# Kernel optimization log

Hardware: AMD Instinct MI355X
Metric: run time of the kernel (lower is better)

The kernel has to match this reference:

```python
import jax, jax.numpy as jnp
import numpy as np

B, H, W = 64, 256, 256
G = 64
V = G * G          # 4096
HID = 512
S = 50


def _conv(x, w, b):
    # x: (B,C,H,W), w: (O,I,3,3) -> 'same' conv, NCHW
    y = jax.lax.conv_general_dilated(x, w, (1, 1), 'SAME',
                                     dimension_numbers=('NCHW', 'OIHW', 'NCHW'))
    return y + b[None, :, None, None]


def setup_inputs() -> dict:
    key = jax.random.key(0)
    ks = jax.random.split(key, 14)

    def lin(k, shape, fan_in):
        return (jax.random.normal(k, shape, jnp.float32) / np.float32(np.sqrt(fan_in)))

    return {
        'mask': jax.random.uniform(ks[0], (B, 1, H, W), jnp.float32),
        'target_ids': jax.random.randint(ks[1], (B, S), 0, V),
        'conv1_w': lin(ks[2], (16, 1, 3, 3), 9), 'conv1_b': jnp.zeros((16,), jnp.float32),
        'conv2_w': lin(ks[3], (32, 16, 3, 3), 16 * 9), 'conv2_b': jnp.zeros((32,), jnp.float32),
        'feat_w': lin(ks[4], (HID, 32), 32), 'feat_b': jnp.zeros((HID,), jnp.float32),
        'ctx_w': lin(ks[5], (HID, HID), HID), 'ctx_b': jnp.zeros((HID,), jnp.float32),
        'tok_emb': jax.random.normal(ks[6], (V + 1, HID), jnp.float32) * 0.02,
        'w_ih': lin(ks[7], (4 * HID, HID), HID), 'w_hh': lin(ks[8], (4 * HID, HID), HID),
        'b_ih': jnp.zeros((4 * HID,), jnp.float32), 'b_hh': jnp.zeros((4 * HID,), jnp.float32),
        'head_w': lin(ks[9], (V, HID), HID), 'head_b': jnp.zeros((V,), jnp.float32),
    }


def reference(mask, target_ids, conv1_w, conv1_b, conv2_w, conv2_b,
              feat_w, feat_b, ctx_w, ctx_b, tok_emb,
              w_ih, w_hh, b_ih, b_hh, head_w, head_b):
    b = mask.shape[0]
    vocab = head_w.shape[0]

    # --- CNN encoder ---
    x = jax.nn.relu(_conv(mask, conv1_w, conv1_b))                    # (B,16,H,W)
    x = jax.lax.reduce_window(x, -jnp.inf, jax.lax.max,
                              (1, 1, 2, 2), (1, 1, 2, 2), 'VALID')    # (B,16,H/2,W/2)
    x = jax.nn.relu(_conv(x, conv2_w, conv2_b))                       # (B,32,H/2,W/2)
    x = x.mean(axis=(2, 3))                                           # AdaptiveAvgPool2d(1) -> (B,32)

    h0 = x @ feat_w.T + feat_b                                        # (B,HID)
    c0 = jnp.zeros_like(h0)
    ctx = h0 @ ctx_w.T + ctx_b                                        # (B,HID)

    # Full teacher forcing (ratio=1.0): input token at t=0 is start token V,
    # at t>0 it is target_ids[:, t-1]. All embeddings gathered upfront.
    start = jnp.full((b, 1), vocab, dtype=target_ids.dtype)
    toks = jnp.concatenate([start, target_ids[:, :-1]], axis=1)       # (B,S)
    embs = tok_emb[toks]                                              # (B,S,HID)
    lstm_in = jnp.swapaxes(embs, 0, 1) + ctx[None]                    # (S,B,HID)

    bias = b_ih + b_hh

    def step(carry, inp):
        h, c = carry
        gates = inp @ w_ih.T + h @ w_hh.T + bias                      # (B,4*HID)
        i, f, g, o = jnp.split(gates, 4, axis=-1)
        c = jax.nn.sigmoid(f) * c + jax.nn.sigmoid(i) * jnp.tanh(g)
        h = jax.nn.sigmoid(o) * jnp.tanh(c)
        logit = h @ head_w.T + head_b                                 # (B,V)
        return (h, c), logit

    _, logits = jax.lax.scan(step, (h0, c0), lstm_in)                 # (S,B,V)
    return jnp.swapaxes(logits, 0, 1)                                 # (B,S,V)
```

## Files before the change

### kernel.cpp

```cpp
#include <hip/hip_runtime.h>
#include <cmath>

typedef __attribute__((ext_vector_type(8))) _Float16 f16x8;
typedef __attribute__((ext_vector_type(2))) _Float16 f16x2;
typedef __attribute__((ext_vector_type(4))) float f32x4;
typedef __attribute__((ext_vector_type(4))) unsigned u32x4;

#define LSTM_NB 32

__device__ __forceinline__ unsigned short f2h(float x) {
  return __builtin_bit_cast(unsigned short, (_Float16)x);
}

__device__ __forceinline__ float dot2(unsigned a, unsigned b, float c) {
#if __has_builtin(__builtin_amdgcn_fdot2)
  return __builtin_amdgcn_fdot2(__builtin_bit_cast(f16x2, a),
                                __builtin_bit_cast(f16x2, b), c, false);
#else
  f16x2 av = __builtin_bit_cast(f16x2, a), bv = __builtin_bit_cast(f16x2, b);
  return fmaf((float)av[0], (float)bv[0], fmaf((float)av[1], (float)bv[1], c));
#endif
}

__device__ __forceinline__ void gload16(const void* g, void* l) {
  __builtin_amdgcn_global_load_lds(
      (const __attribute__((address_space(1))) void*)g,
      (__attribute__((address_space(3))) void*)l, 16, 0, 0);
}

__device__ __forceinline__ void cload16(const void* p, u32x4* dst) {
  asm volatile("global_load_dwordx4 %0, %1, off sc0 sc1"
               : "=v"(*dst)
               : "v"(p));
}

__global__ __launch_bounds__(512) void k_conv(
    const float* __restrict__ mask, const float* __restrict__ w1,
    const float* __restrict__ b1, const float* __restrict__ w2,
    const float* __restrict__ b2, float* __restrict__ part)
{
  __shared__ unsigned s_p1p[8][18 * 36];
  __shared__ unsigned s_w2p[32][8][9];
  __shared__ float s_w1[144];
  __shared__ float s_b1[16];
  __shared__ float s_b2[32];

  const int tid = threadIdx.x;
  const int b = blockIdx.x >> 5;
  const int tile = blockIdx.x & 31;
  const int px0 = (tile & 3) * 32, py0 = (tile >> 2) * 16;
  const float* mb = mask + (size_t)b * 65536;

  for (int i = tid; i < 144; i += 512) s_w1[i] = w1[i];
  for (int i = tid; i < 2304; i += 512) {
    int oc = i / 72, p8 = (i % 72) / 9, k = i % 9;
    unsigned lo = f2h(w2[(size_t)(oc * 16 + 2 * p8) * 9 + k]);
    unsigned hi = f2h(w2[(size_t)(oc * 16 + 2 * p8 + 1) * 9 + k]);
    s_w2p[oc][p8][k] = lo | (hi << 16);
  }
  if (tid < 16) s_b1[tid] = b1[tid];
  if (tid < 32) s_b2[tid] = b2[tid];
  __syncthreads();

  for (int idx = tid; idx < 18 * 34; idx += 512) {
    int ly = idx / 34, lx = idx - ly * 34;
    int py = py0 - 1 + ly, px = px0 - 1 + lx;
    if (py < 0 || py >= 128 || px < 0 || px >= 128) {
      for (int p8 = 0; p8 < 8; p8++) s_p1p[p8][ly * 36 + lx] = 0;
    } else {
      float patch[4][4];
      int gy0 = 2 * py - 1, gx0 = 2 * px - 1;
#pragma unroll
      for (int i = 0; i < 4; i++) {
        int gy = gy0 + i;
        bool yok = (gy >= 0 && gy < 256);
#pragma unroll
        for (int j = 0; j < 4; j++) {
          int gx = gx0 + j;
          patch[i][j] = (yok && gx >= 0 && gx < 256) ? mb[gy * 256 + gx] : 0.f;
        }
      }
      float m[16];
      for (int o = 0; o < 16; o++) {
        float mm = 0.f;
#pragma unroll
        for (int dy = 0; dy < 2; dy++)
#pragma unroll
          for (int dx = 0; dx < 2; dx++) {
            float v = s_b1[o];
#pragma unroll
            for (int ky = 0; ky < 3; ky++)
#pragma unroll
              for (int kx = 0; kx < 3; kx++)
                v = fmaf(patch[dy + ky][dx + kx], s_w1[o * 9 + ky * 3 + kx], v);
            mm = fmaxf(mm, v);
          }
        m[o] = mm;
      }
#pragma unroll
      for (int p8 = 0; p8 < 8; p8++)
        s_p1p[p8][ly * 36 + lx] =
            (unsigned)f2h(m[2 * p8]) | ((unsigned)f2h(m[2 * p8 + 1]) << 16);
    }
  }
  __syncthreads();

  const int ocg = tid >> 6;
  const int sp = tid & 63;
  const int sx = (sp & 7) * 4, sy = (sp >> 3) * 2;
  float acc[4][8];
#pragma unroll
  for (int a = 0; a < 4; a++)
#pragma unroll
    for (int q = 0; q < 8; q++) acc[a][q] = 0.f;

  for (int p8 = 0; p8 < 8; p8++) {
    unsigned pp[4][6];
#pragma unroll
    for (int i = 0; i < 4; i++) {
      const unsigned* row = &s_p1p[p8][(sy + i) * 36 + sx];
#pragma unroll
      for (int j = 0; j < 6; j++) pp[i][j] = row[j];
    }
#pragma unroll
    for (int o4 = 0; o4 < 4; o4++) {
      const unsigned* w = &s_w2p[ocg * 4 + o4][p8][0];
      unsigned w00 = w[0], w01 = w[1], w02 = w[2];
      unsigned w10 = w[3], w11 = w[4], w12 = w[5];
      unsigned w20 = w[6], w21 = w[7], w22 = w[8];
#pragma unroll
      for (int y = 0; y < 2; y++)
#pragma unroll
        for (int x = 0; x < 4; x++) {
          float s = acc[o4][y * 4 + x];
          s = dot2(pp[y][x], w00, s);
          s = dot2(pp[y][x + 1], w01, s);
          s = dot2(pp[y][x + 2], w02, s);
          s = dot2(pp[y + 1][x], w10, s);
          s = dot2(pp[y + 1][x + 1], w11, s);
          s = dot2(pp[y + 1][x + 2], w12, s);
          s = dot2(pp[y + 2][x], w20, s);
          s = dot2(pp[y + 2][x + 1], w21, s);
          s = dot2(pp[y + 2][x + 2], w22, s);
          acc[o4][y * 4 + x] = s;
        }
    }
  }

  const int lane = tid & 63;
#pragma unroll
  for (int o4 = 0; o4 < 4; o4++) {
    float bv = s_b2[ocg * 4 + o4];
    float s = 0.f;
#pragma unroll
    for (int q = 0; q < 8; q++) s += fmaxf(acc[o4][q] + bv, 0.f);
    for (int off = 32; off > 0; off >>= 1) s += __shfl_down(s, off, 64);
    if (lane == 0) part[(b * 32 + tile) * 32 + ocg * 4 + o4] = s;
  }
}

__global__ __launch_bounds__(256) void k_pool_ctx(
    const float* __restrict__ part, const float* __restrict__ feat_w,
    const float* __restrict__ feat_b, const float* __restrict__ ctx_w,
    const float* __restrict__ ctx_b, float* __restrict__ h0,
    unsigned short* __restrict__ h0f, float* __restrict__ ctx)
{
  const int b = blockIdx.x, tid = threadIdx.x;
  __shared__ float pl[32];
  __shared__ float hs[512];
  if (tid < 32) {
    float s = 0.f;
    for (int t = 0; t < 32; t++) s += part[(b * 32 + t) * 32 + tid];
    pl[tid] = s * (1.0f / 16384.0f);
  }
  __syncthreads();
  for (int j = tid; j < 512; j += 256) {
    float acc = feat_b[j];
    const float* w = feat_w + j * 32;
#pragma unroll
    for (int ic = 0; ic < 32; ic++) acc = fmaf(pl[ic], w[ic], acc);
    h0[b * 512 + j] = acc;
    h0f[b * 512 + j] = f2h(acc);
    hs[j] = acc;
  }
  __syncthreads();
  for (int j = tid; j < 512; j += 256) {
    const float* w = ctx_w + (size_t)j * 512;
    float s0 = 0.f, s1 = 0.f, s2 = 0.f, s3 = 0.f;
    for (int k = 0; k < 512; k += 4) {
      float4 w4 = *(const float4*)(w + k);
      s0 = fmaf(hs[k], w4.x, s0);
      s1 = fmaf(hs[k + 1], w4.y, s1);
      s2 = fmaf(hs[k + 2], w4.z, s2);
      s3 = fmaf(hs[k + 3], w4.w, s3);
    }
    ctx[b * 512 + j] = ctx_b[j] + ((s0 + s1) + (s2 + s3));
  }
}

__global__ __launch_bounds__(256) void k_prep(
    const float* __restrict__ wih, const float* __restrict__ hw,
    unsigned short* __restrict__ wihb, unsigned short* __restrict__ hwb,
    int* __restrict__ flags)
{
  const int i = blockIdx.x * 256 + threadIdx.x;
  if (i < 1600) flags[i] = 0;
  if (i < 262144) {
    float4 v = *(const float4*)(wih + (size_t)i * 4);
    unsigned lo = (unsigned)f2h(v.x) | ((unsigned)f2h(v.y) << 16);
    unsigned hi = (unsigned)f2h(v.z) | ((unsigned)f2h(v.w) << 16);
    *(uint2*)(wihb + (size_t)i * 4) = make_uint2(lo, hi);
  } else if (i < 786432) {
    const int j = i - 262144;
    float4 v = *(const float4*)(hw + (size_t)j * 4);
    unsigned lo = (unsigned)f2h(v.x) | ((unsigned)f2h(v.y) << 16);
    unsigned hi = (unsigned)f2h(v.z) | ((unsigned)f2h(v.w) << 16);
    *(uint2*)(hwb + (size_t)j * 4) = make_uint2(lo, hi);
  }
}

__global__ __launch_bounds__(256) void k_zero_f(float* __restrict__ p) {
  p[blockIdx.x * 256 + threadIdx.x] = 0.f;
}

__global__ __launch_bounds__(128) void k_build_A(
    const float* __restrict__ tok_emb, const int* __restrict__ tgt,
    const float* __restrict__ ctx, unsigned short* __restrict__ A)
{
  const int r = blockIdx.x;
  const int t = r >> 6, b = r & 63;
  const int tok = (t == 0) ? 4096 : tgt[b * 50 + (t - 1)];
  const int i = threadIdx.x * 4;
  float4 ev = *(const float4*)(tok_emb + (size_t)tok * 512 + i);
  float4 cv = *(const float4*)(ctx + b * 512 + i);
  unsigned lo = (unsigned)f2h(ev.x + cv.x) | ((unsigned)f2h(ev.y + cv.y) << 16);
  unsigned hi = (unsigned)f2h(ev.z + cv.z) | ((unsigned)f2h(ev.w + cv.w) << 16);
  *(uint2*)(A + (size_t)r * 512 + i) = make_uint2(lo, hi);
}

template <int MODE>
__global__ __launch_bounds__(256) void k_gemm_mfma(
    const unsigned short* __restrict__ A, const unsigned short* __restrict__ B,
    const float* __restrict__ bias_a, const float* __restrict__ bias_b,
    float* __restrict__ C, int NB)
{
  __shared__ unsigned short sA[128 * 32];
  __shared__ unsigned short sB[128 * 32];
  const int tid = threadIdx.x;
  const int bx = blockIdx.x % NB, by = blockIdx.x / NB;
  const int lane = tid & 63, wv = tid >> 6;
  const int wr = wv >> 1, wc = wv & 1;
  const unsigned short* Ab = A + (size_t)by * 128 * 512;
  const unsigned short* Bb = B + (size_t)bx * 128 * 512;

  f32x4 acc[4][4];
#pragma unroll
  for (int m = 0; m < 4; m++)
#pragma unroll
    for (int n = 0; n < 4; n++) acc[m][n] = (f32x4){0.f, 0.f, 0.f, 0.f};

  const int r0 = tid >> 2, c0 = (tid & 3) * 8;
  const int idx1 = tid + 256;
  const int r1 = idx1 >> 2, c1 = (idx1 & 3) * 8;
  unsigned short* lA0 = sA + (size_t)wv * 512;
  unsigned short* lA1 = sA + 2048 + (size_t)wv * 512;
  unsigned short* lB0 = sB + (size_t)wv * 512;
  unsigned short* lB1 = sB + 2048 + (size_t)wv * 512;

  const int frow = lane & 15;
  const int foff = (lane >> 4) * 8;

  for (int kc = 0; kc < 512; kc += 32) {
    gload16(Ab + (size_t)r0 * 512 + kc + c0, lA0);
    gload16(Ab + (size_t)r1 * 512 + kc + c1, lA1);
    gload16(Bb + (size_t)r0 * 512 + kc + c0, lB0);
    gload16(Bb + (size_t)r1 * 512 + kc + c1, lB1);
    __syncthreads();

    f16x8 af[4], bfr[4];
#pragma unroll
    for (int m = 0; m < 4; m++)
      af[m] = *(const f16x8*)(sA + (wr * 64 + m * 16 + frow) * 32 + foff);
#pragma unroll
    for (int n = 0; n < 4; n++)
      bfr[n] = *(const f16x8*)(sB + (wc * 64 + n * 16 + frow) * 32 + foff);
#pragma unroll
    for (int m = 0; m < 4; m++)
#pragma unroll
      for (int n = 0; n < 4; n++)
        acc[m][n] = __builtin_amdgcn_mfma_f32_16x16x32_f16(
            af[m], bfr[n], acc[m][n], 0, 0, 0);
    __syncthreads();
  }

#pragma unroll
  for (int n = 0; n < 4; n++) {
    const int gc = bx * 128 + wc * 64 + n * 16 + (lane & 15);
    const float bv = (MODE == 0) ? (bias_a[gc] + bias_b[gc]) : bias_a[gc];
#pragma unroll
    for (int m = 0; m < 4; m++) {
      const int rb = by * 128 + wr * 64 + m * 16 + (lane >> 4) * 4;
#pragma unroll
      for (int j = 0; j < 4; j++) {
        const int r = rb + j;
        float v = acc[m][n][j] + bv;
        int t = r >> 6, bb = r & 63;
        if (MODE == 0) {
          C[(size_t)t * 131072 + (size_t)gc * 64 + bb] = v;
        } else {
          C[((size_t)bb * 50 + t) * 4096 + gc] = v;
        }
      }
    }
  }
}

__global__ __launch_bounds__(256, 1) void k_lstm_mfma(
    const float* __restrict__ xgT,
    const float* __restrict__ w_hh,
    const unsigned short* __restrict__ h0f,
    unsigned short* __restrict__ hallf,
    int* __restrict__ flags)
{
  __shared__ unsigned short s_h[64 * 512];
  __shared__ float s_g[4][64][17];
  const int tid = threadIdx.x;
  const int kb = blockIdx.x;
  const int g = tid >> 6;
  const int lane = tid & 63;
  const int frow = lane & 15;
  const int foff = (lane >> 4) * 8;

  f16x8 wf[16];
  {
    const float* wrow = w_hh + (size_t)(g * 512 + kb * 16 + frow) * 512;
#pragma unroll
    for (int kf = 0; kf < 16; kf++) {
      float tmp[8];
      *(float4*)tmp = *(const float4*)(wrow + kf * 32 + foff);
      *(float4*)(tmp + 4) = *(const float4*)(wrow + kf * 32 + foff + 4);
#pragma unroll
      for (int j = 0; j < 8; j++) wf[kf][j] = (_Float16)tmp[j];
    }
  }

  float c[4] = {0.f, 0.f, 0.f, 0.f};
  const int b2 = tid & 63, dd2 = tid >> 6;

  for (int t = 0; t < 50; ++t) {
    const unsigned short* H = t ? hallf + (size_t)(t - 1) * 32768 : h0f;

    const float* xr =
        xgT + (size_t)t * 131072 + (size_t)(kb * 16 + dd2 * 4) * 64 + b2;
    float xv[16];
#pragma unroll
    for (int gq = 0; gq < 4; gq++)
#pragma unroll
      for (int i = 0; i < 4; i++)
        xv[gq * 4 + i] = xr[(size_t)(gq * 512 + i) * 64];

    if (t > 0 && tid < 32) {
      while (__hip_atomic_load(&flags[(t - 1) * 32 + tid], __ATOMIC_RELAXED,
                               __HIP_MEMORY_SCOPE_AGENT) == 0) {
        __builtin_amdgcn_s_sleep(1);
      }
    }
    __syncthreads();

    {
      u32x4 r[16];
#pragma unroll
      for (int i = 0; i < 16; i++)
        cload16((const char*)H + (size_t)(tid + i * 256) * 16, &r[i]);
      asm volatile("s_waitcnt vmcnt(0)" ::: "memory");
      __builtin_amdgcn_sched_barrier(0);
#pragma unroll
      for (int i = 0; i < 16; i++) {
        int byte = (tid + i * 256) * 16;
        int swz = byte ^ (((byte >> 10) & 7) << 4);
        *(u32x4*)((char*)s_h + swz) = r[i];
      }
    }
    __syncthreads();

    f32x4 acc[4];
#pragma unroll
    for (int mt = 0; mt < 4; mt++) acc[mt] = (f32x4){0.f, 0.f, 0.f, 0.f};
#pragma unroll
    for (int kf = 0; kf < 16; kf++) {
#pragma unroll
      for (int mt = 0; mt < 4; mt++) {
        const int row = mt * 16 + frow;
        const int byte = (row << 10) + kf * 64 + foff * 2;
        const int swz = byte ^ ((row & 7) << 4);
        f16x8 ah = *(const f16x8*)((const char*)s_h + swz);
        acc[mt] =
            __builtin_amdgcn_mfma_f32_16x16x32_f16(ah, wf[kf], acc[mt], 0, 0, 0);
      }
    }
#pragma unroll
    for (int mt = 0; mt < 4; mt++)
#pragma unroll
      for (int j = 0; j < 4; j++)
        s_g[g][mt * 16 + (lane >> 4) * 4 + j][frow] = acc[mt][j];
    __syncthreads();

    unsigned long long qf = 0;
#pragma unroll
    for (int i = 0; i < 4; i++) {
      float gi = s_g[0][b2][dd2 * 4 + i] + xv[0 + i];
      float gf = s_g[1][b2][dd2 * 4 + i] + xv[4 + i];
      float gg = s_g[2][b2][dd2 * 4 + i] + xv[8 + i];
      float go = s_g[3][b2][dd2 * 4 + i] + xv[12 + i];
      float ig = 1.f / (1.f + expf(-gi));
      float fg = 1.f / (1.f + expf(-gf));
      float og = 1.f / (1.f + expf(-go));
      float gt = tanhf(gg);
      c[i] = fmaf(fg, c[i], ig * gt);
      float h = og * tanhf(c[i]);
      qf |= (unsigned long long)f2h(h) << (16 * i);
    }
    const size_t ho = (size_t)b2 * 512 + kb * 16 + dd2 * 4;
    __hip_atomic_store((unsigned long long*)(hallf + (size_t)t * 32768 + ho),
                       qf, __ATOMIC_RELAXED, __HIP_MEMORY_SCOPE_AGENT);
    __syncthreads();
    if (t < 49 && tid == 0)
      __hip_atomic_store(&flags[t * 32 + kb], 1, __ATOMIC_RELAXED,
                         __HIP_MEMORY_SCOPE_AGENT);
  }
}

__global__ __launch_bounds__(256) void k_lstm_step1(
    const float* __restrict__ xgT, const float* __restrict__ w_hh,
    const float* __restrict__ hin, float* __restrict__ hout,
    unsigned short* __restrict__ hallf_t, float* __restrict__ cbuf, int t)
{
  __shared__ float s_w[8][512];
  __shared__ float s_g[2][4][64];
  const int tid = threadIdx.x;
  const int dd0 = blockIdx.x * 2;

  for (int idx = tid; idx < 1024; idx += 256) {
    int row = idx >> 7;
    int k4 = (idx & 127) << 2;
    int q_ = row >> 1, dd_i = row & 1;
    *(float4*)&s_w[row][k4] =
        *(const float4*)(w_hh + (size_t)(q_ * 512 + dd0 + dd_i) * 512 + k4);
  }
  const int b = tid & 63;
  const int q = tid >> 6;
  __syncthreads();

  const float* hc = hin + b * 512;
  const float* xr = xgT + (size_t)t * 131072 + (size_t)(q * 512 + dd0) * 64 + b;
  float a0 = xr[0], a1 = xr[64];
  const float* w0 = s_w[q * 2 + 0];
  const float* w1 = s_w[q * 2 + 1];
#pragma unroll 8
  for (int k = 0; k < 512; k += 4) {
    float4 h4 = *(const float4*)(hc + k);
    float4 u = *(const float4*)(w0 + k);
    float4 v = *(const float4*)(w1 + k);
    a0 = fmaf(h4.x, u.x, fmaf(h4.y, u.y, fmaf(h4.z, u.z, fmaf(h4.w, u.w, a0))));
    a1 = fmaf(h4.x, v.x, fmaf(h4.y, v.y, fmaf(h4.z, v.z, fmaf(h4.w, v.w, a1))));
  }
  s_g[0][q][b] = a0;
  s_g[1][q][b] = a1;
  __syncthreads();
  if (q < 2) {
    const int dd = dd0 + q;
    float gi = s_g[q][0][b], gf = s_g[q][1][b];
    float gg = s_g[q][2][b], go = s_g[q][3][b];
    float ig = 1.f / (1.f + expf(-gi));
    float fg = 1.f / (1.f + expf(-gf));
    float og = 1.f / (1.f + expf(-go));
    float gt = tanhf(gg);
    float c = fmaf(fg, cbuf[b * 512 + dd], ig * gt);
    float h = og * tanhf(c);
    cbuf[b * 512 + dd] = c;
    hout[b * 512 + dd] = h;
    hallf_t[(size_t)b * 512 + dd] = f2h(h);
  }
}

extern "C" void kernel_launch(void* const* d_in, const int* in_sizes, int n_in,
                              void* d_out, int out_size, void* d_ws,
                              size_t ws_size, hipStream_t stream) {
  const float* mask   = (const float*)d_in[0];
  const int*   tgt    = (const int*)d_in[1];
  const float* w1     = (const float*)d_in[2];
  const float* b1     = (const float*)d_in[3];
  const float* w2     = (const float*)d_in[4];
  const float* b2     = (const float*)d_in[5];
  const float* feat_w = (const float*)d_in[6];
  const float* feat_b = (const float*)d_in[7];
  const float* ctx_w  = (const float*)d_in[8];
  const float* ctx_b  = (const float*)d_in[9];
  const float* temb   = (const float*)d_in[10];
  const float* w_ih   = (const float*)d_in[11];
  const float* w_hh_p = (const float*)d_in[12];
  const float* b_ih   = (const float*)d_in[13];
  const float* b_hh   = (const float*)d_in[14];
  const float* head_w = (const float*)d_in[15];
  const float* head_b = (const float*)d_in[16];

  float* ws = (float*)d_ws;
  float* part  = ws;
  float* hbuf  = ws + 65536;
  float* ctx   = ws + 131072;
  int*   flags = (int*)(ws + 163840);
  unsigned short* h0f  = (unsigned short*)(ws + 165440);
  unsigned short* Ab16 = (unsigned short*)(ws + 181824);
  unsigned short* hallf = Ab16;
  unsigned short* wihb = (unsigned short*)(ws + 1001024);
  unsigned short* hwb  = (unsigned short*)(ws + 1525312);
  float* xgT   = ws + 2573888;
  float* cbuf  = part;
  float* out   = (float*)d_out;

  k_conv<<<2048, 512, 0, stream>>>(mask, w1, b1, w2, b2, part);
  k_prep<<<3072, 256, 0, stream>>>(w_ih, head_w, wihb, hwb, flags);
  k_pool_ctx<<<64, 256, 0, stream>>>(part, feat_w, feat_b, ctx_w, ctx_b,
                                     hbuf, h0f, ctx);
  k_build_A<<<3200, 128, 0, stream>>>(temb, tgt, ctx, Ab16);
  k_gemm_mfma<0><<<25 * 16, 256, 0, stream>>>(Ab16, wihb, b_ih, b_hh, xgT, 16);

  {
    const float* xgT_c = xgT;
    const float* whh_c = w_hh_p;
    const unsigned short* h0f_c = h0f;
    unsigned short* hallf_c = hallf;
    int* flags_c = flags;
    void* args[] = {(void*)&xgT_c, (void*)&whh_c, (void*)&h0f_c,
                    (void*)&hallf_c, (void*)&flags_c};
    hipError_t e = hipLaunchCooperativeKernel(
        (const void*)k_lstm_mfma, dim3(LSTM_NB), dim3(256), args, 0, stream);
    if (e != hipSuccess) {
      (void)hipGetLastError();
      k_zero_f<<<128, 256, 0, stream>>>(cbuf);
      for (int t = 0; t < 50; t++) {
        const float* hin = hbuf + (t & 1) * 32768;
        float* hout = hbuf + ((t + 1) & 1) * 32768;
        k_lstm_step1<<<256, 256, 0, stream>>>(
            xgT, w_hh_p, hin, hout, hallf + (size_t)t * 32768, cbuf, t);
      }
    }
  }

  k_gemm_mfma<1><<<25 * 32, 256, 0, stream>>>(hallf, hwb, head_b, nullptr, out, 32);
}
```

Baseline: 510.6 us.

## Fuse weight prep into conv kernel, stage mask tile in LDS, reorder hidden-state layout

Folds the fp16 weight-conversion work into extra blocks of the conv launch, removing one kernel launch. The conv now stages the mask tile once into LDS as fp16 instead of each thread reading overlapping global patches. It also changes the stored hidden-state layout to batch-major (b, t, hid), so the head GEMM writes its output rows contiguously without index remapping. The cost is strided gathers inside the LSTM recurrence, and the mask is rounded to fp16 before conv1.

After: 534.2 us. 4.6% more time.

```diff
diff --git a/kernel.cpp b/kernel.cpp
--- a/kernel.cpp
+++ b/kernel.cpp
@@ -7,6 +7,8 @@
 typedef __attribute__((ext_vector_type(4))) unsigned u32x4;
 
 #define LSTM_NB 32
+#define CONV_NB 2048
+#define PREP_NB 1536
 
 __device__ __forceinline__ unsigned short f2h(float x) {
   return __builtin_bit_cast(unsigned short, (_Float16)x);
@@ -37,8 +39,12 @@
 __global__ __launch_bounds__(512) void k_conv(
     const float* __restrict__ mask, const float* __restrict__ w1,
     const float* __restrict__ b1, const float* __restrict__ w2,
-    const float* __restrict__ b2, float* __restrict__ part)
+    const float* __restrict__ b2, float* __restrict__ part,
+    const float* __restrict__ wih, const float* __restrict__ hw,
+    unsigned short* __restrict__ wihb, unsigned short* __restrict__ hwb,
+    int* __restrict__ flags)
 {
+  __shared__ unsigned short s_mask[38 * 72];
   __shared__ unsigned s_p1p[8][18 * 36];
   __shared__ unsigned s_w2p[32][8][9];
   __shared__ float s_w1[144];
@@ -46,10 +52,30 @@
   __shared__ float s_b2[32];
 
   const int tid = threadIdx.x;
+
+  if (blockIdx.x >= CONV_NB) {
+    const int i = (blockIdx.x - CONV_NB) * 512 + tid;
+    if (i < 6400) flags[i] = 0;
+    if (i < 262144) {
+      float4 v = *(const float4*)(wih + (size_t)i * 4);
+      unsigned lo = (unsigned)f2h(v.x) | ((unsigned)f2h(v.y) << 16);
+      unsigned hi = (unsigned)f2h(v.z) | ((unsigned)f2h(v.w) << 16);
+      *(uint2*)(wihb + (size_t)i * 4) = make_uint2(lo, hi);
+    } else {
+      const int j = i - 262144;
+      float4 v = *(const float4*)(hw + (size_t)j * 4);
+      unsigned lo = (unsigned)f2h(v.x) | ((unsigned)f2h(v.y) << 16);
+      unsigned hi = (unsigned)f2h(v.z) | ((unsigned)f2h(v.w) << 16);
+      *(uint2*)(hwb + (size_t)j * 4) = make_uint2(lo, hi);
+    }
+    return;
+  }
+
   const int b = blockIdx.x >> 5;
   const int tile = blockIdx.x & 31;
   const int px0 = (tile & 3) * 32, py0 = (tile >> 2) * 16;
   const float* mb = mask + (size_t)b * 65536;
+  const int gr0 = 2 * py0 - 3, gc0 = 2 * px0 - 3;
 
   for (int i = tid; i < 144; i += 512) s_w1[i] = w1[i];
   for (int i = tid; i < 2304; i += 512) {
@@ -60,6 +86,14 @@
   }
   if (tid < 16) s_b1[tid] = b1[tid];
   if (tid < 32) s_b2[tid] = b2[tid];
+
+  for (int idx = tid; idx < 38 * 70; idx += 512) {
+    int r = idx / 70, cc = idx - r * 70;
+    int gr = gr0 + r, gc = gc0 + cc;
+    float v = (gr >= 0 && gr < 256 && gc >= 0 && gc < 256)
+                  ? mb[gr * 256 + gc] : 0.f;
+    s_mask[r * 72 + cc] = f2h(v);
+  }
   __syncthreads();
 
   for (int idx = tid; idx < 18 * 34; idx += 512) {
@@ -69,17 +103,12 @@
       for (int p8 = 0; p8 < 8; p8++) s_p1p[p8][ly * 36 + lx] = 0;
     } else {
       float patch[4][4];
-      int gy0 = 2 * py - 1, gx0 = 2 * px - 1;
-#pragma unroll
-      for (int i = 0; i < 4; i++) {
-        int gy = gy0 + i;
-        bool yok = (gy >= 0 && gy < 256);
-#pragma unroll
-        for (int j = 0; j < 4; j++) {
-          int gx = gx0 + j;
-          patch[i][j] = (yok && gx >= 0 && gx < 256) ? mb[gy * 256 + gx] : 0.f;
-        }
-      }
+      const unsigned short* pm = &s_mask[(2 * ly) * 72 + 2 * lx];
+#pragma unroll
+      for (int i = 0; i < 4; i++)
+#pragma unroll
+        for (int j = 0; j < 4; j++)
+          patch[i][j] = (float)__builtin_bit_cast(_Float16, pm[i * 72 + j]);
       float m[16];
       for (int o = 0; o < 16; o++) {
         float mm = 0.f;
@@ -195,27 +224,6 @@
       s3 = fmaf(hs[k + 3], w4.w, s3);
     }
     ctx[b * 512 + j] = ctx_b[j] + ((s0 + s1) + (s2 + s3));
-  }
-}
-
-__global__ __launch_bounds__(256) void k_prep(
-    const float* __restrict__ wih, const float* __restrict__ hw,
-    unsigned short* __restrict__ wihb, unsigned short* __restrict__ hwb,
-    int* __restrict__ flags)
-{
-  const int i = blockIdx.x * 256 + threadIdx.x;
-  if (i < 1600) flags[i] = 0;
-  if (i < 262144) {
-    float4 v = *(const float4*)(wih + (size_t)i * 4);
-    unsigned lo = (unsigned)f2h(v.x) | ((unsigned)f2h(v.y) << 16);
-    unsigned hi = (unsigned)f2h(v.z) | ((unsigned)f2h(v.w) << 16);
-    *(uint2*)(wihb + (size_t)i * 4) = make_uint2(lo, hi);
-  } else if (i < 786432) {
-    const int j = i - 262144;
-    float4 v = *(const float4*)(hw + (size_t)j * 4);
-    unsigned lo = (unsigned)f2h(v.x) | ((unsigned)f2h(v.y) << 16);
-    unsigned hi = (unsigned)f2h(v.z) | ((unsigned)f2h(v.w) << 16);
-    *(uint2*)(hwb + (size_t)j * 4) = make_uint2(lo, hi);
   }
 }
 
@@ -304,11 +312,11 @@
       for (int j = 0; j < 4; j++) {
         const int r = rb + j;
         float v = acc[m][n][j] + bv;
-        int t = r >> 6, bb = r & 63;
         if (MODE == 0) {
+          int t = r >> 6, bb = r & 63;
           C[(size_t)t * 131072 + (size_t)gc * 64 + bb] = v;
         } else {
-          C[((size_t)bb * 50 + t) * 4096 + gc] = v;
+          C[(size_t)r * 4096 + gc] = v;
         }
       }
     }
@@ -348,8 +356,6 @@
   const int b2 = tid & 63, dd2 = tid >> 6;
 
   for (int t = 0; t < 50; ++t) {
-    const unsigned short* H = t ? hallf + (size_t)(t - 1) * 32768 : h0f;
-
     const float* xr =
         xgT + (size_t)t * 131072 + (size_t)(kb * 16 + dd2 * 4) * 64 + b2;
     float xv[16];
@@ -369,9 +375,19 @@
 
     {
       u32x4 r[16];
-#pragma unroll
-      for (int i = 0; i < 16; i++)
-        cload16((const char*)H + (size_t)(tid + i * 256) * 16, &r[i]);
+      if (t == 0) {
+#pragma unroll
+        for (int i = 0; i < 16; i++)
+          cload16((const char*)h0f + (size_t)(tid + i * 256) * 16, &r[i]);
+      } else {
+        const char* base = (const char*)(hallf + (size_t)(t - 1) * 512);
+#pragma unroll
+        for (int i = 0; i < 16; i++) {
+          int idx = tid + i * 256;
+          int row = idx >> 6, ch = idx & 63;
+          cload16(base + (size_t)row * 51200 + ch * 16, &r[i]);
+        }
+      }
       asm volatile("s_waitcnt vmcnt(0)" ::: "memory");
       __builtin_amdgcn_sched_barrier(0);
 #pragma unroll
@@ -420,9 +436,9 @@
       float h = og * tanhf(c[i]);
       qf |= (unsigned long long)f2h(h) << (16 * i);
     }
-    const size_t ho = (size_t)b2 * 512 + kb * 16 + dd2 * 4;
-    __hip_atomic_store((unsigned long long*)(hallf + (size_t)t * 32768 + ho),
-                       qf, __ATOMIC_RELAXED, __HIP_MEMORY_SCOPE_AGENT);
+    const size_t ho = ((size_t)b2 * 50 + t) * 512 + kb * 16 + dd2 * 4;
+    __hip_atomic_store((unsigned long long*)(hallf + ho), qf,
+                       __ATOMIC_RELAXED, __HIP_MEMORY_SCOPE_AGENT);
     __syncthreads();
     if (t < 49 && tid == 0)
       __hip_atomic_store(&flags[t * 32 + kb], 1, __ATOMIC_RELAXED,
@@ -433,7 +449,7 @@
 __global__ __launch_bounds__(256) void k_lstm_step1(
     const float* __restrict__ xgT, const float* __restrict__ w_hh,
     const float* __restrict__ hin, float* __restrict__ hout,
-    unsigned short* __restrict__ hallf_t, float* __restrict__ cbuf, int t)
+    unsigned short* __restrict__ hallf, float* __restrict__ cbuf, int t)
 {
   __shared__ float s_w[8][512];
   __shared__ float s_g[2][4][64];
@@ -479,7 +495,7 @@
     float h = og * tanhf(c);
     cbuf[b * 512 + dd] = c;
     hout[b * 512 + dd] = h;
-    hallf_t[(size_t)b * 512 + dd] = f2h(h);
+    hallf[((size_t)b * 50 + t) * 512 + dd] = f2h(h);
   }
 }
 
@@ -509,17 +525,17 @@
   float* hbuf  = ws + 65536;
   float* ctx   = ws + 131072;
   int*   flags = (int*)(ws + 163840);
-  unsigned short* h0f  = (unsigned short*)(ws + 165440);
-  unsigned short* Ab16 = (unsigned short*)(ws + 181824);
+  unsigned short* h0f  = (unsigned short*)(ws + 170240);
+  unsigned short* Ab16 = (unsigned short*)(ws + 186624);
   unsigned short* hallf = Ab16;
-  unsigned short* wihb = (unsigned short*)(ws + 1001024);
-  unsigned short* hwb  = (unsigned short*)(ws + 1525312);
-  float* xgT   = ws + 2573888;
+  unsigned short* wihb = (unsigned short*)(ws + 1005824);
+  unsigned short* hwb  = (unsigned short*)(ws + 1530112);
+  float* xgT   = ws + 2578688;
   float* cbuf  = part;
   float* out   = (float*)d_out;
 
-  k_conv<<<2048, 512, 0, stream>>>(mask, w1, b1, w2, b2, part);
-  k_prep<<<3072, 256, 0, stream>>>(w_ih, head_w, wihb, hwb, flags);
+  k_conv<<<CONV_NB + PREP_NB, 512, 0, stream>>>(
+      mask, w1, b1, w2, b2, part, w_ih, head_w, wihb, hwb, flags);
   k_pool_ctx<<<64, 256, 0, stream>>>(part, feat_w, feat_b, ctx_w, ctx_b,
                                      hbuf, h0f, ctx);
   k_build_A<<<3200, 128, 0, stream>>>(temb, tgt, ctx, Ab16);
@@ -542,7 +558,7 @@
         const float* hin = hbuf + (t & 1) * 32768;
         float* hout = hbuf + ((t + 1) & 1) * 32768;
         k_lstm_step1<<<256, 256, 0, stream>>>(
-            xgT, w_hh_p, hin, hout, hallf + (size_t)t * 32768, cbuf, t);
+            xgT, w_hh_p, hin, hout, hallf, cbuf, t);
       }
     }
   }
```
